# Kernel optimization log

Measured on AMD Instinct MI355X. Metric: run time of the kernel, lower is better.

Reference implementation:

```python
import jax, jax.numpy as jnp
import numpy as np
import math

HIDDEN = 1024
N_HEADS = 16
HEAD_DIM = HIDDEN // N_HEADS  # 64
B, S = 4, 8192


def setup_inputs() -> dict:
    key = jax.random.key(0)
    ks = jax.random.split(key, 5)
    scale = 1.0 / math.sqrt(HIDDEN)
    return {
        "hidden_states": jax.random.normal(ks[0], (B, S, HIDDEN), dtype=jnp.float32),
        "Wq": jax.random.normal(ks[1], (HIDDEN, HIDDEN), dtype=jnp.float32) * scale,
        "Wk": jax.random.normal(ks[2], (HIDDEN, HIDDEN), dtype=jnp.float32) * scale,
        "Wv": jax.random.normal(ks[3], (HIDDEN, HIDDEN), dtype=jnp.float32) * scale,
        "Wo": jax.random.normal(ks[4], (HIDDEN, HIDDEN), dtype=jnp.float32) * scale,
    }


def reference(hidden_states, Wq, Wk, Wv, Wo):
    b, s, _ = hidden_states.shape
    # nn.Linear(bias=False): y = x @ W.T
    q = (hidden_states @ Wq.T).reshape(b, s, N_HEADS, HEAD_DIM)
    k = (hidden_states @ Wk.T).reshape(b, s, N_HEADS, HEAD_DIM)
    v = (hidden_states @ Wv.T).reshape(b, s, N_HEADS, HEAD_DIM)
    # Faithful to source: NO transpose to (b,h,s,d); matmul contracts head_dim
    # per (batch, position), yielding [b, s, h, h] head-mixing weights.
    attn = jnp.einsum("bshd,bstd->bsht", q, k) / math.sqrt(HEAD_DIM)
    attn = jax.nn.softmax(attn, axis=-1)
    out = jnp.einsum("bsht,bstd->bshd", attn, v).reshape(b, s, HIDDEN)
    return out @ Wo.T
```

## Files before the change

### kernel.cpp

```cpp
#include <hip/hip_runtime.h>
#include <hip/hip_bf16.h>


typedef short bf16x8 __attribute__((ext_vector_type(8)));
typedef float f32x4  __attribute__((ext_vector_type(4)));

__device__ __forceinline__ float bf2f(short u) {
    union { unsigned int ui; float f; } cv;
    cv.ui = ((unsigned int)(unsigned short)u) << 16;
    return cv.f;
}
__device__ __forceinline__ short f2bf(float f) {
    __hip_bfloat16 h = __float2bfloat16(f);
    return *reinterpret_cast<short*>(&h);
}

__device__ __forceinline__ void gload_lds16(const void* g, void* lds) {
    const unsigned __attribute__((address_space(1)))* gp =
        reinterpret_cast<const unsigned __attribute__((address_space(1)))*>((unsigned long long)g);
    unsigned __attribute__((address_space(3)))* lp =
        reinterpret_cast<unsigned __attribute__((address_space(3)))*>(
            (unsigned int)(unsigned long long)lds);
    __builtin_amdgcn_global_load_lds(gp, lp, 16, 0, 0);
}

__global__ void detect_dtype(const unsigned* __restrict__ x, int* __restrict__ flag) {
    __shared__ int cnt;
    if (threadIdx.x == 0) cnt = 0;
    __syncthreads();
    int c = 0;
    for (int i = threadIdx.x; i < 4096; i += 256) {
        const unsigned u = x[(long)i * 4001 + 3];
        const unsigned b = (u >> 7) & 0xFF;
        c += (b >= 0x70 && b <= 0x87) ? 1 : 0;
    }
    atomicAdd(&cnt, c);
    __syncthreads();
    if (threadIdx.x == 0) *flag = (cnt > 2048) ? 0 : 1;
}

__global__ void convert_any(const void* __restrict__ src, long eoff,
                            short* __restrict__ dst, long n,
                            const int* __restrict__ flag) {
    const int f = *flag;
    const long step = (long)gridDim.x * blockDim.x * 8;
    for (long i = ((long)blockIdx.x * blockDim.x + threadIdx.x) * 8; i < n; i += step) {
        if (f) {
            const float* s = (const float*)src + eoff + i;
            const f32x4 a = *(const f32x4*)s;
            const f32x4 b = *(const f32x4*)(s + 4);
            bf16x8 o;
            o[0] = f2bf(a[0]); o[1] = f2bf(a[1]); o[2] = f2bf(a[2]); o[3] = f2bf(a[3]);
            o[4] = f2bf(b[0]); o[5] = f2bf(b[1]); o[6] = f2bf(b[2]); o[7] = f2bf(b[3]);
            *(bf16x8*)(dst + i) = o;
        } else {
            *(bf16x8*)(dst + i) = *(const bf16x8*)((const short*)src + eoff + i);
        }
    }
}

__device__ __forceinline__ void gemm256_core(const short* __restrict__ A,
                                             const short* __restrict__ W,
                                             void* __restrict__ C,
                                             const int* flag_fp32,
                                             long m0, int n0, short* lds) {
    constexpr int K = 1024, N = 1024;
    const int tid  = threadIdx.x;
    const int lane = tid & 63;
    const int wid  = tid >> 6;
    const int wm = wid >> 2, wn = wid & 3;

    short* A0 = lds;
    short* B0 = lds + 16384;
    short* A1 = lds + 32768;
    short* B1 = lds + 49152;

    const int srl = tid >> 3;
    const int kcs = (tid & 7) ^ (srl & 7);
    int aoff[4], boff[4];
    #pragma unroll
    for (int i = 0; i < 4; ++i) {
        const int row = i * 64 + srl;
        aoff[i] = (int)((m0 + row) * K + kcs * 8);
        boff[i] = (n0 + row) * K + kcs * 8;
    }
    const int ldsw = wid * 512;

    auto STAGE = [&](short* bA, short* bB, int t) {
        const int kadd = t * 64;
        #pragma unroll
        for (int i = 0; i < 4; ++i)
            gload_lds16(A + aoff[i] + kadd, bA + i * 4096 + ldsw);
        #pragma unroll
        for (int i = 0; i < 4; ++i)
            gload_lds16(W + boff[i] + kadd, bB + i * 4096 + ldsw);
    };

    f32x4 acc[8][4] = {};

    auto COMPUTE = [&](const short* bA, const short* bB) {
        #pragma unroll
        for (int ks = 0; ks < 2; ++ks) {
            const int kx8 = (((ks * 4 + (lane >> 4)) ^ (lane & 7))) * 8;
            bf16x8 af[8], bfr[4];
            #pragma unroll
            for (int mf = 0; mf < 8; ++mf)
                af[mf] = *(const bf16x8*)(bA + (wm * 128 + mf * 16 + (lane & 15)) * 64 + kx8);
            #pragma unroll
            for (int nf = 0; nf < 4; ++nf)
                bfr[nf] = *(const bf16x8*)(bB + (wn * 64 + nf * 16 + (lane & 15)) * 64 + kx8);
            __builtin_amdgcn_s_setprio(1);
            #pragma unroll
            for (int mf = 0; mf < 8; ++mf)
                #pragma unroll
                for (int nf = 0; nf < 4; ++nf)
                    acc[mf][nf] = __builtin_amdgcn_mfma_f32_16x16x32_bf16(
                                      af[mf], bfr[nf], acc[mf][nf], 0, 0, 0);
            __builtin_amdgcn_s_setprio(0);
        }
    };

    STAGE(A0, B0, 0);
    STAGE(A1, B1, 1);

    for (int tt = 0; tt < 7; ++tt) {
        const int t = tt * 2;
        asm volatile("s_waitcnt vmcnt(8)" ::: "memory");
        __builtin_amdgcn_s_barrier();
        asm volatile("" ::: "memory");
        COMPUTE(A0, B0);
        asm volatile("" ::: "memory");
        __builtin_amdgcn_s_barrier();
        STAGE(A0, B0, t + 2);
        asm volatile("s_waitcnt vmcnt(8)" ::: "memory");
        __builtin_amdgcn_s_barrier();
        asm volatile("" ::: "memory");
        COMPUTE(A1, B1);
        asm volatile("" ::: "memory");
        __builtin_amdgcn_s_barrier();
        STAGE(A1, B1, t + 3);
    }
    asm volatile("s_waitcnt vmcnt(8)" ::: "memory");
    __builtin_amdgcn_s_barrier();
    asm volatile("" ::: "memory");
    COMPUTE(A0, B0);
    asm volatile("s_waitcnt vmcnt(0)" ::: "memory");
    __builtin_amdgcn_s_barrier();
    asm volatile("" ::: "memory");
    COMPUTE(A1, B1);

    const int f = flag_fp32 ? *flag_fp32 : 0;
    #pragma unroll
    for (int mf = 0; mf < 8; ++mf) {
        #pragma unroll
        for (int nf = 0; nf < 4; ++nf) {
            const int  col   = n0 + wn * 64 + nf * 16 + (lane & 15);
            const long rbase = m0 + wm * 128 + mf * 16 + (lane >> 4) * 4;
            if (f) {
                float* Cf = (float*)C;
                #pragma unroll
                for (int r = 0; r < 4; ++r)
                    Cf[(rbase + r) * N + col] = acc[mf][nf][r];
            } else {
                short* Cs = (short*)C;
                #pragma unroll
                for (int r = 0; r < 4; ++r)
                    Cs[(rbase + r) * N + col] = f2bf(acc[mf][nf][r]);
            }
        }
    }
}

__global__ __launch_bounds__(512, 2) void gemm_qkv256(const short* __restrict__ A,
                                                      const short* __restrict__ W0,
                                                      const short* __restrict__ W1,
                                                      const short* __restrict__ W2,
                                                      short* __restrict__ C0,
                                                      short* __restrict__ C1,
                                                      short* __restrict__ C2) {
    __shared__ __align__(16) short lds[65536];
    const int nwg = gridDim.x;
    const int q8  = nwg >> 3;
    const int d   = blockIdx.x;
    const int lin = (d & 7) * q8 + (d >> 3);
    const int x   = lin / 12;
    const int r   = lin - x * 12;
    const int y   = r >> 2;
    const int yy  = r / 3;
    const int z   = r - yy * 3;
    (void)y;
    const short* W = (z == 0) ? W0 : (z == 1) ? W1 : W2;
    short*       C = (z == 0) ? C0 : (z == 1) ? C1 : C2;
    gemm256_core(A, W, C, nullptr, (long)x * 256, yy * 256, lds);
}

__global__ __launch_bounds__(512, 2) void gemm_out256(const short* __restrict__ A,
                                                      const short* __restrict__ W,
                                                      void* __restrict__ C,
                                                      long moff,
                                                      const int* __restrict__ flag) {
    __shared__ __align__(16) short lds[65536];
    const int nwg = gridDim.x;
    const int q8  = nwg >> 3;
    const int d   = blockIdx.x;
    const int lin = (d & 7) * q8 + (d >> 3);
    const int x   = lin >> 2;
    const int yy  = lin & 3;
    gemm256_core(A, W, C, flag, moff + (long)x * 256, yy * 256, lds);
}

__global__ __launch_bounds__(256) void attn_mix(const short* __restrict__ Q,
                                                const short* __restrict__ K,
                                                const short* __restrict__ V,
                                                short* __restrict__ Z) {
    constexpr int RS = 72;
    __shared__ short sq[4][16 * RS];
    __shared__ short sk[4][16 * RS];
    __shared__ short sv[4][16 * RS];
    __shared__ float sp[4][256];

    const int  tid  = threadIdx.x;
    const int  lane = tid & 63;
    const int  w    = tid >> 6;
    const long tok  = (long)blockIdx.x * 4 + w;

    const short* qg = Q + tok * 1024;
    const short* kg = K + tok * 1024;
    const short* vg = V + tok * 1024;

    #pragma unroll
    for (int it = 0; it < 2; ++it) {
        const int c   = lane + 64 * it;
        const int row = c >> 3;
        const int cc  = (c & 7) * 8;
        *(bf16x8*)&sq[w][row * RS + cc] = *(const bf16x8*)(qg + c * 8);
        *(bf16x8*)&sk[w][row * RS + cc] = *(const bf16x8*)(kg + c * 8);
        *(bf16x8*)&sv[w][row * RS + cc] = *(const bf16x8*)(vg + c * 8);
    }
    __syncthreads();

    const int h  = lane >> 2;
    const int t0 = (lane & 3) * 4;
    float sc[4] = {0.f, 0.f, 0.f, 0.f};
    for (int d = 0; d < 64; ++d) {
        const float qv = bf2f(sq[w][h * RS + d]);
        #pragma unroll
        for (int j = 0; j < 4; ++j)
            sc[j] += qv * bf2f(sk[w][(t0 + j) * RS + d]);
    }
    #pragma unroll
    for (int j = 0; j < 4; ++j) sc[j] *= 0.125f;

    float mx = fmaxf(fmaxf(sc[0], sc[1]), fmaxf(sc[2], sc[3]));
    mx = fmaxf(mx, __shfl_xor(mx, 1));
    mx = fmaxf(mx, __shfl_xor(mx, 2));
    float ex[4], s = 0.f;
    #pragma unroll
    for (int j = 0; j < 4; ++j) { ex[j] = __expf(sc[j] - mx); s += ex[j]; }
    s += __shfl_xor(s, 1);
    s += __shfl_xor(s, 2);
    const float inv = 1.f / s;
    #pragma unroll
    for (int j = 0; j < 4; ++j) sp[w][h * 16 + t0 + j] = ex[j] * inv;
    __syncthreads();

    const int dbase = (lane & 3) * 16;
    float o[16] = {};
    for (int t = 0; t < 16; ++t) {
        const float p = sp[w][h * 16 + t];
        const bf16x8 v0 = *(const bf16x8*)&sv[w][t * RS + dbase];
        const bf16x8 v1 = *(const bf16x8*)&sv[w][t * RS + dbase + 8];
        #pragma unroll
        for (int e = 0; e < 8; ++e) {
            o[e]     += p * bf2f(v0[e]);
            o[e + 8] += p * bf2f(v1[e]);
        }
    }
    bf16x8 ov0, ov1;
    #pragma unroll
    for (int e = 0; e < 8; ++e) { ov0[e] = f2bf(o[e]); ov1[e] = f2bf(o[e + 8]); }
    *(bf16x8*)(Z + tok * 1024 + lane * 16)     = ov0;
    *(bf16x8*)(Z + tok * 1024 + lane * 16 + 8) = ov1;
}

extern "C" void kernel_launch(void* const* d_in, const int* in_sizes, int n_in,
                              void* d_out, int out_size, void* d_ws, size_t ws_size,
                              hipStream_t stream) {
    const void* X = d_in[0];

    const long TOT = 32768;
    constexpr long WELEM = 1024 * 1024;

    char* ws   = (char*)d_ws;
    int*  flag = (int*)ws;
    short* Wqb = (short*)(ws + 256);
    short* Wkb = Wqb + WELEM;
    short* Wvb = Wkb + WELEM;
    short* Wob = Wvb + WELEM;
    short* dyn = Wob + WELEM;

    const size_t fixed = 256 + 4 * WELEM * 2;
    long chunk = 256;
    const long tiers[4] = {32768, 8192, 2048, 512};
    for (int i = 0; i < 4; ++i)
        if (fixed + (size_t)6 * tiers[i] * 1024 * 2 <= ws_size) { chunk = tiers[i]; break; }

    short* Xb = dyn;
    short* Qb = Xb + chunk * 1024;
    short* Kb = Qb + chunk * 1024;
    short* Vb = Kb + chunk * 1024;
    short* Zb = Vb + chunk * 1024;

    detect_dtype<<<1, 256, 0, stream>>>((const unsigned*)X, flag);
    convert_any<<<512, 256, 0, stream>>>(d_in[1], 0, Wqb, WELEM, flag);
    convert_any<<<512, 256, 0, stream>>>(d_in[2], 0, Wkb, WELEM, flag);
    convert_any<<<512, 256, 0, stream>>>(d_in[3], 0, Wvb, WELEM, flag);
    convert_any<<<512, 256, 0, stream>>>(d_in[4], 0, Wob, WELEM, flag);

    for (long t0 = 0; t0 < TOT; t0 += chunk) {
        convert_any<<<2048, 256, 0, stream>>>(X, t0 * 1024, Xb, chunk * 1024, flag);
        gemm_qkv256<<<dim3((chunk / 256) * 12), 512, 0, stream>>>(Xb, Wqb, Wkb, Wvb,
                                                                  Qb, Kb, Vb);
        attn_mix<<<dim3(chunk / 4), 256, 0, stream>>>(Qb, Kb, Vb, Zb);
        gemm_out256<<<dim3((chunk / 256) * 4), 512, 0, stream>>>(Zb - t0 * 1024, Wob,
                                                                 d_out, t0, flag);
    }
}
```

Baseline: 429.7 us.

## Interleave global-to-LDS prefetch with MFMA quarters in GEMM main loop

Restructures the 256x256 GEMM K-loop from a two-stage prefetch-ahead scheme into a single-prefetch ping-pong loop. Each K-tile's compute is split into four quarters, and each quarter issues a slice of the next tile's global-to-LDS loads. The aim is to spread memory traffic across the MFMA work instead of bursting it. The cost is prefetch depth dropping from two tiles to one, plus more barriers per tile (eight instead of two), which may expose load latency.

```diff
diff --git a/kernel.cpp b/kernel.cpp
--- a/kernel.cpp
+++ b/kernel.cpp
@@ -86,68 +86,65 @@
     }
     const int ldsw = wid * 512;
 
-    auto STAGE = [&](short* bA, short* bB, int t) {
-        const int kadd = t * 64;
+    f32x4 acc[8][4] = {};
+
+    #pragma unroll
+    for (int i = 0; i < 4; ++i) gload_lds16(A + aoff[i], A0 + i * 4096 + ldsw);
+    #pragma unroll
+    for (int i = 0; i < 4; ++i) gload_lds16(W + boff[i], B0 + i * 4096 + ldsw);
+
+    for (int t = 0; t < 16; ++t) {
+        const int cur = t & 1;
+        const short* rA = cur ? A1 : A0;
+        const short* rB = cur ? B1 : B0;
+        short* sA = cur ? A0 : A1;
+        short* sB = cur ? B0 : B1;
+        const int kadd = (t + 1) * 64;
+        const bool more = (t < 15);
+
         #pragma unroll
-        for (int i = 0; i < 4; ++i)
-            gload_lds16(A + aoff[i] + kadd, bA + i * 4096 + ldsw);
-        #pragma unroll
-        for (int i = 0; i < 4; ++i)
-            gload_lds16(W + boff[i] + kadd, bB + i * 4096 + ldsw);
-    };
-
-    f32x4 acc[8][4] = {};
-
-    auto COMPUTE = [&](const short* bA, const short* bB) {
-        #pragma unroll
-        for (int ks = 0; ks < 2; ++ks) {
-            const int kx8 = (((ks * 4 + (lane >> 4)) ^ (lane & 7))) * 8;
-            bf16x8 af[8], bfr[4];
+        for (int q = 0; q < 4; ++q) {
+            if (more) {
+                if (q == 0) {
+                    gload_lds16(A + aoff[0] + kadd, sA + 0 * 4096 + ldsw);
+                    gload_lds16(A + aoff[1] + kadd, sA + 1 * 4096 + ldsw);
+                } else if (q == 1) {
+                    gload_lds16(A + aoff[2] + kadd, sA + 2 * 4096 + ldsw);
+                    gload_lds16(A + aoff[3] + kadd, sA + 3 * 4096 + ldsw);
+                } else if (q == 2) {
+                    gload_lds16(W + boff[0] + kadd, sB + 0 * 4096 + ldsw);
+                    gload_lds16(W + boff[1] + kadd, sB + 1 * 4096 + ldsw);
+                } else {
+                    gload_lds16(W + boff[2] + kadd, sB + 2 * 4096 + ldsw);
+                    gload_lds16(W + boff[3] + kadd, sB + 3 * 4096 + ldsw);
+                }
+            }
+            if (q == 0) {
+                if (more) asm volatile("s_waitcnt vmcnt(2)" ::: "memory");
+                else      asm volatile("s_waitcnt vmcnt(0)" ::: "memory");
+            }
+            __builtin_amdgcn_s_barrier();
+            __builtin_amdgcn_sched_barrier(0);
+            const int mfh = q >> 1, ks = q & 1;
+            const int kx8 = ((ks * 4 + (lane >> 4)) ^ (lane & 7)) * 8;
+            bf16x8 af[4], bfr[4];
             #pragma unroll
-            for (int mf = 0; mf < 8; ++mf)
-                af[mf] = *(const bf16x8*)(bA + (wm * 128 + mf * 16 + (lane & 15)) * 64 + kx8);
+            for (int m = 0; m < 4; ++m)
+                af[m] = *(const bf16x8*)(rA + (wm * 128 + (mfh * 4 + m) * 16 + (lane & 15)) * 64 + kx8);
             #pragma unroll
-            for (int nf = 0; nf < 4; ++nf)
-                bfr[nf] = *(const bf16x8*)(bB + (wn * 64 + nf * 16 + (lane & 15)) * 64 + kx8);
+            for (int n = 0; n < 4; ++n)
+                bfr[n] = *(const bf16x8*)(rB + (wn * 64 + n * 16 + (lane & 15)) * 64 + kx8);
             __builtin_amdgcn_s_setprio(1);
             #pragma unroll
-            for (int mf = 0; mf < 8; ++mf)
+            for (int m = 0; m < 4; ++m)
                 #pragma unroll
-                for (int nf = 0; nf < 4; ++nf)
-                    acc[mf][nf] = __builtin_amdgcn_mfma_f32_16x16x32_bf16(
-                                      af[mf], bfr[nf], acc[mf][nf], 0, 0, 0);
+                for (int n = 0; n < 4; ++n)
+                    acc[mfh * 4 + m][n] = __builtin_amdgcn_mfma_f32_16x16x32_bf16(
+                                              af[m], bfr[n], acc[mfh * 4 + m][n], 0, 0, 0);
             __builtin_amdgcn_s_setprio(0);
+            __builtin_amdgcn_s_barrier();
         }
-    };
-
-    STAGE(A0, B0, 0);
-    STAGE(A1, B1, 1);
-
-    for (int tt = 0; tt < 7; ++tt) {
-        const int t = tt * 2;
-        asm volatile("s_waitcnt vmcnt(8)" ::: "memory");
-        __builtin_amdgcn_s_barrier();
-        asm volatile("" ::: "memory");
-        COMPUTE(A0, B0);
-        asm volatile("" ::: "memory");
-        __builtin_amdgcn_s_barrier();
-        STAGE(A0, B0, t + 2);
-        asm volatile("s_waitcnt vmcnt(8)" ::: "memory");
-        __builtin_amdgcn_s_barrier();
-        asm volatile("" ::: "memory");
-        COMPUTE(A1, B1);
-        asm volatile("" ::: "memory");
-        __builtin_amdgcn_s_barrier();
-        STAGE(A1, B1, t + 3);
-    }
-    asm volatile("s_waitcnt vmcnt(8)" ::: "memory");
-    __builtin_amdgcn_s_barrier();
-    asm volatile("" ::: "memory");
-    COMPUTE(A0, B0);
-    asm volatile("s_waitcnt vmcnt(0)" ::: "memory");
-    __builtin_amdgcn_s_barrier();
-    asm volatile("" ::: "memory");
-    COMPUTE(A1, B1);
+    }
 
     const int f = flag_fp32 ? *flag_fp32 : 0;
     #pragma unroll
@@ -185,10 +182,8 @@
     const int lin = (d & 7) * q8 + (d >> 3);
     const int x   = lin / 12;
     const int r   = lin - x * 12;
-    const int y   = r >> 2;
     const int yy  = r / 3;
     const int z   = r - yy * 3;
-    (void)y;
     const short* W = (z == 0) ? W0 : (z == 1) ? W1 : W2;
     short*       C = (z == 0) ? C0 : (z == 1) ? C1 : C2;
     gemm256_core(A, W, C, nullptr, (long)x * 256, yy * 256, lds);
```

After: 415.5 us. 3.3% less time.
